# Kernel tuning notes

Measured on AMD Instinct MI355X. Metric: run time of the kernel, lower is better.

Reference implementation:

```python
import jax, jax.numpy as jnp
import numpy as np

NHEAD = 4
NLAYERS = 4
C = 128
EPS = 1e-5


def ln(x, g, b):
    m = x.mean(-1, keepdims=True)
    v = jnp.var(x, axis=-1, keepdims=True)
    return (x - m) / jnp.sqrt(v + EPS) * g + b


def mha_rel(q_in, k_in, in_w, in_b, out_w, out_b, pos_enc, pos_idx, self_attn):
    # q_in/k_in: [W, N, C]; pos_enc: [2W-1, C]; pos_idx: [W*W] int
    w, bsz, c = q_in.shape
    hd = c // NHEAD
    scale = hd ** -0.5
    if self_attn:
        qkv = q_in @ in_w.T + in_b
        q, k, v = jnp.split(qkv, 3, axis=-1)
    else:
        q = q_in @ in_w[:c].T + in_b[:c]
        kv = k_in @ in_w[c:].T + in_b[c:]
        k, v = jnp.split(kv, 2, axis=-1)
    pe = pos_enc[pos_idx].reshape(w, w, c)             # [W, W', C] gathered rel-pos
    qr_kr = pe @ in_w[:2 * c].T + in_b[:2 * c]
    q_r, k_r = jnp.split(qr_kr, 2, axis=-1)
    q = (q * scale).reshape(w, bsz, NHEAD, hd)
    q_r = (q_r * scale).reshape(w, w, NHEAD, hd)
    k = k.reshape(w, bsz, NHEAD, hd)
    v = v.reshape(w, bsz, NHEAD, hd)
    k_r = k_r.reshape(w, w, NHEAD, hd)
    # content-content + content-pos + pos-content (STTR MultiheadAttentionRelative)
    attn = (jnp.einsum('wnec,vnec->newv', q, k)
            + jnp.einsum('wnec,wvec->newv', q, k_r)
            + jnp.einsum('vnec,wvec->newv', k, q_r))   # [N, E, W, W']
    raw = attn.sum(1)
    a = jax.nn.softmax(attn, axis=-1)
    v_o = jnp.einsum('newv,vnec->wnec', a, v).reshape(w, bsz, c)
    v_o = v_o @ out_w.T + out_b
    return v_o, a.sum(1) / NHEAD, raw


def _forward(feat_left, feat_right, pos_enc,
             s_iw, s_ib, s_ow, s_ob, s_g, s_b,
             c_iw, c_ib, c_ow, c_ob, c_g1, c_b1, c_g2, c_b2):
    bs, c, hn0, w = feat_left.shape
    hn = hn0 * bs

    def to_seq(x):  # [bs,c,hn,w] -> [w, hn*bs, c]
        return jnp.transpose(jnp.transpose(x, (1, 3, 2, 0)).reshape(c, w, hn), (1, 2, 0))

    fl = to_seq(feat_left)
    fr = to_seq(feat_right)
    pos_idx = (jnp.arange(w - 1, -1, -1)[:, None] + jnp.arange(w)[None, :]).reshape(-1)
    pos_flip = pos_enc[::-1]
    feat = jnp.concatenate([fl, fr], axis=1)           # [w, 2hn, c]
    for i in range(NLAYERS):
        # self attention over concatenated left/right
        f2 = ln(feat, s_g[i], s_b[i])
        f2, _, _ = mha_rel(f2, f2, s_iw[i], s_ib[i], s_ow[i], s_ob[i], pos_enc, pos_idx, True)
        feat = feat + f2
        # cross attention
        fl, fr = feat[:, :hn], feat[:, hn:]
        fl2 = ln(fl, c_g1[i], c_b1[i])
        fr2 = ln(fr, c_g1[i], c_b1[i])
        fr2u, _, _ = mha_rel(fr2, fl2, c_iw[i], c_ib[i], c_ow[i], c_ob[i], pos_flip, pos_idx, False)
        fr = fr + fr2u
        fr2n = ln(fr, c_g2[i], c_b2[i])
        fl2u, _, _ = mha_rel(fl2, fr2n, c_iw[i], c_ib[i], c_ow[i], c_ob[i], pos_enc, pos_idx, False)
        fl = fl + fl2u
        feat = jnp.concatenate([fl, fr], axis=1)
    return feat


def setup_inputs() -> dict:
    key = jax.random.key(0)
    ks = jax.random.split(key, 20)
    bs, hn, w = 2, 64, 192
    p = 0.02
    return {
        "feat_left": jax.random.normal(ks[0], (bs, C, hn, w), jnp.float32),
        "feat_right": jax.random.normal(ks[1], (bs, C, hn, w), jnp.float32),
        "pos_enc": jax.random.normal(ks[2], (2 * w - 1, C), jnp.float32),
        "s_iw": jax.random.normal(ks[3], (NLAYERS, 3 * C, C), jnp.float32) * p,
        "s_ib": jax.random.normal(ks[4], (NLAYERS, 3 * C), jnp.float32) * p,
        "s_ow": jax.random.normal(ks[5], (NLAYERS, C, C), jnp.float32) * p,
        "s_ob": jax.random.normal(ks[6], (NLAYERS, C), jnp.float32) * p,
        "s_g": jnp.ones((NLAYERS, C), jnp.float32),
        "s_b": jnp.zeros((NLAYERS, C), jnp.float32),
        "c_iw": jax.random.normal(ks[7], (NLAYERS, 3 * C, C), jnp.float32) * p,
        "c_ib": jax.random.normal(ks[8], (NLAYERS, 3 * C), jnp.float32) * p,
        "c_ow": jax.random.normal(ks[9], (NLAYERS, C, C), jnp.float32) * p,
        "c_ob": jax.random.normal(ks[10], (NLAYERS, C), jnp.float32) * p,
        "c_g1": jnp.ones((NLAYERS, C), jnp.float32),
        "c_b1": jnp.zeros((NLAYERS, C), jnp.float32),
        "c_g2": jnp.ones((NLAYERS, C), jnp.float32),
        "c_b2": jnp.zeros((NLAYERS, C), jnp.float32),
    }


def reference(feat_left, feat_right, pos_enc,
              s_iw, s_ib, s_ow, s_ob, s_g, s_b,
              c_iw, c_ib, c_ow, c_ob, c_g1, c_b1, c_g2, c_b2):
    return _forward(feat_left, feat_right, pos_enc,
                    s_iw, s_ib, s_ow, s_ob, s_g, s_b,
                    c_iw, c_ib, c_ow, c_ob, c_g1, c_b1, c_g2, c_b2)
```

## Files before the change

kernel.cpp:

```cpp
#include <hip/hip_runtime.h>
#include <hip/hip_bf16.h>
#include <math.h>

#define WW 192
#define NTOT 256
#define HNN 128
#define CC 128
#define NH 4
#define NLAY 4
#define EPSF 1e-5f
#define SCALE 0.17677669529663687f

typedef __attribute__((ext_vector_type(8))) short short8_t;
typedef __attribute__((ext_vector_type(4))) float f32x4;

#define MFMA(a, b, c) __builtin_amdgcn_mfma_f32_16x16x32_bf16(a, b, c, 0, 0, 0)

__device__ __forceinline__ ushort f2b(float f) {
  union { float f; uint u; } x; x.f = f;
  uint r = x.u + 0x7fffu + ((x.u >> 16) & 1u);
  return (ushort)(r >> 16);
}

__global__ __launch_bounds__(256) void k_build_feat(const float* __restrict__ L,
                                                    const float* __restrict__ R,
                                                    float* __restrict__ feat) {
  __shared__ float tile[32][33];
  int wt = blockIdx.x, h0 = blockIdx.y, z = blockIdx.z;
  int ct = z & 3, b = (z >> 2) & 1, side = z >> 3;
  const float* src = side ? R : L;
  int tx = threadIdx.x & 31, ty = threadIdx.x >> 5;
  const float* sp = src + ((size_t)(b * 128 + ct * 32) * 64 + h0) * 192 + wt * 32;
  #pragma unroll
  for (int yy = 0; yy < 4; ++yy) {
    int c = ty * 4 + yy;
    tile[c][tx] = sp[(size_t)c * 64 * 192 + tx];
  }
  __syncthreads();
  int n = 2 * h0 + b + side * 128;
  #pragma unroll
  for (int yy = 0; yy < 4; ++yy) {
    int w = ty * 4 + yy;
    feat[((size_t)(wt * 32 + w) * 256 + n) * 128 + ct * 32 + tx] = tile[tx][w];
  }
}

__global__ __launch_bounds__(256) void k_wconv(
    const float* __restrict__ s_iw, const float* __restrict__ s_ow,
    const float* __restrict__ c_iw, const float* __restrict__ c_ow,
    ushort* __restrict__ out) {
  int i4 = (blockIdx.x * 256 + threadIdx.x) * 4;
  const float* src;
  int off;
  if (i4 < 196608) { src = s_iw; off = i4; }
  else if (i4 < 262144) { src = s_ow; off = i4 - 196608; }
  else if (i4 < 458752) { src = c_iw; off = i4 - 262144; }
  else { src = c_ow; off = i4 - 458752; }
  float4 v = *(const float4*)(src + off);
  ushort4 o;
  o.x = f2b(v.x); o.y = f2b(v.y); o.z = f2b(v.z); o.w = f2b(v.w);
  *(ushort4*)(out + i4) = o;
}

__global__ __launch_bounds__(256) void k_ln(const float* __restrict__ src,
                                            ushort* __restrict__ dst,
                                            const float* __restrict__ g,
                                            const float* __restrict__ b,
                                            int n0, int nsub) {
  int t = blockIdx.x * 4 + (threadIdx.x >> 6);
  int lane = threadIdx.x & 63;
  int w = t / nsub, h = t - w * nsub;
  size_t row = (size_t)(w * NTOT + n0 + h) * CC;
  int c0 = lane * 2;
  float2 x = *(const float2*)(src + row + c0);
  float s = x.x + x.y;
  float s2 = x.x * x.x + x.y * x.y;
  #pragma unroll
  for (int o = 1; o < 64; o <<= 1) {
    s += __shfl_xor(s, o);
    s2 += __shfl_xor(s2, o);
  }
  float m = s * (1.0f / 128.0f);
  float var = s2 * (1.0f / 128.0f) - m * m;
  float inv = rsqrtf(var + EPSF);
  float oa = (x.x - m) * inv * g[c0] + b[c0];
  float ob = (x.y - m) * inv * g[c0 + 1] + b[c0 + 1];
  uint pack = (uint)f2b(oa) | ((uint)f2b(ob) << 16);
  *(uint*)(dst + row + c0) = pack;
}

__global__ __launch_bounds__(256) void k_gemm_bf16(
    const ushort* __restrict__ X, int xN, int x0,
    const ushort* __restrict__ Wb, const float* __restrict__ bias,
    void* __restrict__ Yv, int yN, int y0, int ystride, int yf32res,
    int T, int nsub, float* __restrict__ Ymir) {
  extern __shared__ char smem[];
  ushort* As = (ushort*)smem;
  ushort* Bs = As + 128 * 128;
  float* biasS = (float*)(Bs + 128 * 128);

  int bm = blockIdx.x, bn = blockIdx.y;
  int tid = threadIdx.x;

  {
    int row = tid >> 1;
    int ce0 = (tid & 1) * 64;
    int t = bm * 128 + row;
    bool ok = (t < T);
    int w = 0, h = 0;
    if (ok) { w = t / nsub; h = t - w * nsub; }
    const ushort* src = X + (size_t)(w * xN + x0 + h) * CC + ce0;
    #pragma unroll
    for (int i = 0; i < 8; ++i) {
      short8_t v = {};
      if (ok) v = *(const short8_t*)(src + i * 8);
      int cb = (ce0 + i * 8) * 2;
      *(short8_t*)((char*)As + row * 256 + (cb ^ ((row & 7) << 4))) = v;
    }
    const ushort* wsrc = Wb + (size_t)(bn * 128 + row) * CC + ce0;
    #pragma unroll
    for (int i = 0; i < 8; ++i) {
      short8_t v = *(const short8_t*)(wsrc + i * 8);
      int cb = (ce0 + i * 8) * 2;
      *(short8_t*)((char*)Bs + row * 256 + (cb ^ ((row & 7) << 4))) = v;
    }
    if (tid < 128) biasS[tid] = bias[bn * 128 + tid];
  }
  __syncthreads();

  int lane = tid & 63, wid = tid >> 6;
  int wm = (wid >> 1) * 64, wn = (wid & 1) * 64;
  int r = lane & 15, g = lane >> 4;

  f32x4 acc[4][4] = {};
  #pragma unroll
  for (int kc = 0; kc < 4; ++kc) {
    short8_t af[4], bf[4];
    #pragma unroll
    for (int mt = 0; mt < 4; ++mt) {
      int row = wm + mt * 16 + r;
      af[mt] = *(const short8_t*)((const char*)As + row * 256 + ((kc * 64 + g * 16) ^ ((row & 7) << 4)));
    }
    #pragma unroll
    for (int nt = 0; nt < 4; ++nt) {
      int row = wn + nt * 16 + r;
      bf[nt] = *(const short8_t*)((const char*)Bs + row * 256 + ((kc * 64 + g * 16) ^ ((row & 7) << 4)));
    }
    __builtin_amdgcn_s_setprio(1);
    #pragma unroll
    for (int mt = 0; mt < 4; ++mt)
      #pragma unroll
      for (int nt = 0; nt < 4; ++nt)
        acc[mt][nt] = MFMA(af[mt], bf[nt], acc[mt][nt]);
    __builtin_amdgcn_s_setprio(0);
  }

  #pragma unroll
  for (int mt = 0; mt < 4; ++mt) {
    #pragma unroll
    for (int reg = 0; reg < 4; ++reg) {
      int t = bm * 128 + wm + mt * 16 + g * 4 + reg;
      if (t < T) {
        int w = t / nsub, h = t - w * nsub;
        size_t ybase = (size_t)(w * yN + y0 + h) * ystride + bn * 128;
        #pragma unroll
        for (int nt = 0; nt < 4; ++nt) {
          int nn = wn + nt * 16 + r;
          float v = acc[mt][nt][reg] + biasS[nn];
          if (yf32res) {
            float nv = ((float*)Yv)[ybase + nn] + v;
            ((float*)Yv)[ybase + nn] = nv;
            if (Ymir) Ymir[ybase + nn] = nv;
          } else {
            ((ushort*)Yv)[ybase + nn] = f2b(v);
          }
        }
      }
    }
  }
}

__global__ __launch_bounds__(256) void k_rr(
    const float* __restrict__ pos_enc,
    const float* __restrict__ s_iw, const float* __restrict__ s_ib,
    const float* __restrict__ c_iw, const float* __restrict__ c_ib,
    ushort* __restrict__ out_all) {
  extern __shared__ char smem[];
  ushort* As = (ushort*)smem;
  ushort* Bs = As + 128 * 128;
  float* biasS = (float*)(Bs + 128 * 128);

  int bm = blockIdx.x, bn = blockIdx.y, z = blockIdx.z;
  int layer = z >> 1;
  const float* Wt = ((z & 1) ? c_iw : s_iw) + (size_t)layer * 384 * CC;
  const float* bias = ((z & 1) ? c_ib : s_ib) + layer * 384;
  ushort* out = out_all + (size_t)z * 383 * 256;
  int tid = threadIdx.x;

  {
    int row = tid >> 1;
    int ce0 = (tid & 1) * 64;
    int t = bm * 128 + row;
    bool ok = (t < 383);
    const float* src = pos_enc + (size_t)t * CC + ce0;
    #pragma unroll
    for (int i = 0; i < 8; ++i) {
      float4 v0 = ok ? *(const float4*)(src + i * 8) : make_float4(0.f, 0.f, 0.f, 0.f);
      float4 v1 = ok ? *(const float4*)(src + i * 8 + 4) : make_float4(0.f, 0.f, 0.f, 0.f);
      short8_t pv;
      pv[0] = (short)f2b(v0.x); pv[1] = (short)f2b(v0.y);
      pv[2] = (short)f2b(v0.z); pv[3] = (short)f2b(v0.w);
      pv[4] = (short)f2b(v1.x); pv[5] = (short)f2b(v1.y);
      pv[6] = (short)f2b(v1.z); pv[7] = (short)f2b(v1.w);
      int cb = (ce0 + i * 8) * 2;
      *(short8_t*)((char*)As + row * 256 + (cb ^ ((row & 7) << 4))) = pv;
    }
    const float* wsrc = Wt + (size_t)(bn * 128 + row) * CC + ce0;
    #pragma unroll
    for (int i = 0; i < 8; ++i) {
      float4 v0 = *(const float4*)(wsrc + i * 8);
      float4 v1 = *(const float4*)(wsrc + i * 8 + 4);
      short8_t pv;
      pv[0] = (short)f2b(v0.x); pv[1] = (short)f2b(v0.y);
      pv[2] = (short)f2b(v0.z); pv[3] = (short)f2b(v0.w);
      pv[4] = (short)f2b(v1.x); pv[5] = (short)f2b(v1.y);
      pv[6] = (short)f2b(v1.z); pv[7] = (short)f2b(v1.w);
      int cb = (ce0 + i * 8) * 2;
      *(short8_t*)((char*)Bs + row * 256 + (cb ^ ((row & 7) << 4))) = pv;
    }
    if (tid < 128) biasS[tid] = bias[bn * 128 + tid];
  }
  __syncthreads();

  int lane = tid & 63, wid = tid >> 6;
  int wm = (wid >> 1) * 64, wn = (wid & 1) * 64;
  int r = lane & 15, g = lane >> 4;

  f32x4 acc[4][4] = {};
  #pragma unroll
  for (int kc = 0; kc < 4; ++kc) {
    short8_t af[4], bf[4];
    #pragma unroll
    for (int mt = 0; mt < 4; ++mt) {
      int row = wm + mt * 16 + r;
      af[mt] = *(const short8_t*)((const char*)As + row * 256 + ((kc * 64 + g * 16) ^ ((row & 7) << 4)));
    }
    #pragma unroll
    for (int nt = 0; nt < 4; ++nt) {
      int row = wn + nt * 16 + r;
      bf[nt] = *(const short8_t*)((const char*)Bs + row * 256 + ((kc * 64 + g * 16) ^ ((row & 7) << 4)));
    }
    #pragma unroll
    for (int mt = 0; mt < 4; ++mt)
      #pragma unroll
      for (int nt = 0; nt < 4; ++nt)
        acc[mt][nt] = MFMA(af[mt], bf[nt], acc[mt][nt]);
  }

  #pragma unroll
  for (int mt = 0; mt < 4; ++mt) {
    #pragma unroll
    for (int reg = 0; reg < 4; ++reg) {
      int t = bm * 128 + wm + mt * 16 + g * 4 + reg;
      if (t < 383) {
        #pragma unroll
        for (int nt = 0; nt < 4; ++nt) {
          int nn = wn + nt * 16 + r;
          out[(size_t)t * 256 + bn * 128 + nn] = f2b(acc[mt][nt][reg] + biasS[nn]);
        }
      }
    }
  }
}

#define KS_ST 36
#define VT_ST 196
#define B2_ST 37
#define PL_ST 20

template <int SGN>
__global__ __launch_bounds__(256, 4) void k_attn_mfma(
    const ushort* __restrict__ qbuf, int qstride, int qoff, int qN, int qn0,
    const ushort* __restrict__ kvbuf, int kvstride, int koff, int voff, int kN, int kn0,
    const ushort* __restrict__ rrb,
    ushort* __restrict__ obuf, int oN,
    int nblk) {
  __shared__ ushort Ks[192 * KS_ST];
  __shared__ ushort Vt[32 * VT_ST];
  __shared__ float Sb[4 * 16 * B2_ST];
  __shared__ uint PLb[4 * 16 * PL_ST];

  int bid = blockIdx.x;
  int n = bid % nblk;
  int rest = bid / nblk;
  int h = rest & 3;
  int ts = rest >> 2;
  int tid = threadIdx.x;
  int lane = tid & 63, wid = tid >> 6;
  int r = lane & 15, g = lane >> 4;
  int g4 = g * 4;

  for (int i = tid; i < 768; i += 256) {
    int row = i >> 2, c8 = (i & 3) * 8;
    *(short8_t*)&Ks[row * KS_ST + c8] =
        *(const short8_t*)(kvbuf + (size_t)(row * kN + kn0 + n) * kvstride + koff + h * 32 + c8);
  }
  {
    uint* Vtu = (uint*)Vt;
    for (int i = tid; i < 384; i += 256) {
      int dg = i / 96;
      int p = i - dg * 96;
      const ushort* vb = kvbuf + (size_t)((2 * p) * kN + kn0 + n) * kvstride + voff + h * 32 + dg * 8;
      short8_t a = *(const short8_t*)vb;
      short8_t b = *(const short8_t*)(vb + (size_t)kN * kvstride);
      #pragma unroll
      for (int j = 0; j < 8; ++j)
        Vtu[(dg * 8 + j) * 98 + p] = ((uint)(ushort)a[j]) | (((uint)(ushort)b[j]) << 16);
    }
  }
  int w0 = (ts * 4 + wid) * 16;
  short8_t qf = *(const short8_t*)(qbuf + (size_t)((w0 + r) * qN + qn0 + n) * qstride + qoff + h * 32 + g * 8);
  __syncthreads();

  float* flat = Sb + wid * 16 * B2_ST;
  uint* PL = PLb + wid * 16 * PL_ST;
  const ushort* KRg = rrb + 128 + h * 32 + g * 8;
  const ushort* QRg = rrb + h * 32 + g * 8;
  const f32x4 zf = {0.f, 0.f, 0.f, 0.f};

  int ca = (SGN < 0) ? (r + 1) : (31 - r);
  int cbn = (SGN < 0) ? (17 + r) : (15 - r);
  int rdcol = 16 - r + g4;

  f32x4 esum = zf, o0 = zf, o1 = zf;

  #pragma unroll
  for (int vp = 0; vp < 6; ++vp) {
    #pragma unroll
    for (int half = 0; half < 2; ++half) {
      int s = 2 * vp + half;
      int v0 = s * 16;
      short8_t kf = *(const short8_t*)&Ks[(v0 + r) * KS_ST + g * 8];
      int base2 = 176 + SGN * (w0 - v0);
      const ushort* krp = KRg + (size_t)(base2 + r) * 256;
      const ushort* qrp = QRg + (size_t)(base2 + r) * 256;
      short8_t krf0 = *(const short8_t*)krp;
      short8_t krf1 = *(const short8_t*)(krp + 16 * 256);
      short8_t qrf0 = *(const short8_t*)qrp;
      short8_t qrf1 = *(const short8_t*)(qrp + 16 * 256);
      __builtin_amdgcn_s_setprio(1);
      f32x4 t1  = MFMA(kf, qf, zf);
      f32x4 t3a = MFMA(kf, qrf0, zf);
      f32x4 t3b = MFMA(kf, qrf1, zf);
      f32x4 t2a = MFMA(qf, krf0, zf);
      f32x4 t2b = MFMA(qf, krf1, zf);
      __builtin_amdgcn_s_setprio(0);
      #pragma unroll
      for (int reg = 0; reg < 4; ++reg) {
        flat[(g4 + reg) * B2_ST + ca] = t2a[reg];
        flat[(g4 + reg) * B2_ST + cbn] = t2b[reg];
      }
      f32x4 p2v = *(const f32x4*)&flat[r * B2_ST + rdcol];
      f32x4 ev;
      #pragma unroll
      for (int reg = 0; reg < 4; ++reg) {
        int js = 15 + SGN * (r - g4 - reg);
        int idx = (lane & 48) | (js & 15);
        float v3a = __shfl(t3a[reg], idx);
        float v3b = __shfl(t3b[reg], idx);
        float p3 = (js < 16) ? v3a : v3b;
        float e = __expf((t1[reg] + p2v[reg] + p3) * SCALE);
        ev[reg] = e;
        esum[reg] += e;
      }
      uint pa = (uint)f2b(ev[0]) | ((uint)f2b(ev[1]) << 16);
      uint pbu = (uint)f2b(ev[2]) | ((uint)f2b(ev[3]) << 16);
      *(uint2*)&PL[r * PL_ST + 8 * half + 2 * g] = make_uint2(pa, pbu);
    }
    union { uint u[4]; short8_t s8; } pb;
    uint4 pr = *(const uint4*)&PL[r * PL_ST + 4 * g];
    pb.u[0] = pr.x; pb.u[1] = pr.y; pb.u[2] = pr.z; pb.u[3] = pr.w;
    short8_t vt0 = *(const short8_t*)&Vt[r * VT_ST + vp * 32 + g * 8];
    short8_t vt1 = *(const short8_t*)&Vt[(16 + r) * VT_ST + vp * 32 + g * 8];
    __builtin_amdgcn_s_setprio(1);
    o0 = MFMA(vt0, pb.s8, o0);
    o1 = MFMA(vt1, pb.s8, o1);
    __builtin_amdgcn_s_setprio(0);
  }

  float ssum = (esum[0] + esum[1]) + (esum[2] + esum[3]);
  ssum += __shfl_xor(ssum, 16);
  ssum += __shfl_xor(ssum, 32);

  float inv = 1.0f / ssum;
  ushort4 u0, u1;
  u0.x = f2b(o0[0] * inv); u0.y = f2b(o0[1] * inv);
  u0.z = f2b(o0[2] * inv); u0.w = f2b(o0[3] * inv);
  u1.x = f2b(o1[0] * inv); u1.y = f2b(o1[1] * inv);
  u1.z = f2b(o1[2] * inv); u1.w = f2b(o1[3] * inv);
  size_t rowb = (size_t)((w0 + r) * oN + n) * CC + h * 32;
  *(ushort4*)(obuf + rowb + g4) = u0;
  *(ushort4*)(obuf + rowb + 16 + g4) = u1;
}

extern "C" void kernel_launch(void* const* d_in, const int* in_sizes, int n_in,
                              void* d_out, int out_size, void* d_ws, size_t ws_size,
                              hipStream_t stream) {
  const float* feat_left  = (const float*)d_in[0];
  const float* feat_right = (const float*)d_in[1];
  const float* pos_enc    = (const float*)d_in[2];
  const float* s_iw = (const float*)d_in[3];
  const float* s_ib = (const float*)d_in[4];
  const float* s_ow = (const float*)d_in[5];
  const float* s_ob = (const float*)d_in[6];
  const float* s_g  = (const float*)d_in[7];
  const float* s_b  = (const float*)d_in[8];
  const float* c_iw = (const float*)d_in[9];
  const float* c_ib = (const float*)d_in[10];
  const float* c_ow = (const float*)d_in[11];
  const float* c_ob = (const float*)d_in[12];
  const float* c_g1 = (const float*)d_in[13];
  const float* c_b1 = (const float*)d_in[14];
  const float* c_g2 = (const float*)d_in[15];
  const float* c_b2 = (const float*)d_in[16];

  char* W = (char*)d_ws;
  const int FEAT_N = WW * NTOT * CC;
  float*  feat    = (float*)W;
  ushort* f2obuf  = (ushort*)(W + 25165824);
  ushort* qkv     = (ushort*)(W + 37748736);
  ushort* kv2     = (ushort*)(W + 75497472);
  ushort* rrb_all = (ushort*)(W + 88080384);
  ushort* wbf     = (ushort*)(W + 89649152);

  ushort* f2   = f2obuf;
  ushort* obuf = f2obuf;

  const int GEMM_LDS = 128 * 128 * 2 * 2 + 128 * 4;
  hipFuncSetAttribute(reinterpret_cast<const void*>(&k_gemm_bf16),
                      hipFuncAttributeMaxDynamicSharedMemorySize, GEMM_LDS);
  hipFuncSetAttribute(reinterpret_cast<const void*>(&k_rr),
                      hipFuncAttributeMaxDynamicSharedMemorySize, GEMM_LDS);

  k_build_feat<<<dim3(6, 64, 16), 256, 0, stream>>>(feat_left, feat_right, feat);
  k_rr<<<dim3(3, 2, 8), 256, GEMM_LDS, stream>>>(pos_enc, s_iw, s_ib, c_iw, c_ib, rrb_all);
  k_wconv<<<512, 256, 0, stream>>>(s_iw, s_ow, c_iw, c_ow, wbf);

  const ushort* siw_bf_base = wbf;
  const ushort* sow_bf_base = wbf + 196608;
  const ushort* ciw_bf_base = wbf + 262144;
  const ushort* cow_bf_base = wbf + 458752;

  const int T_FULL = WW * NTOT;
  const int T_HALF = WW * HNN;

  for (int i = 0; i < NLAY; ++i) {
    const float* sib = s_ib + i * 384;
    const float* sob = s_ob + i * CC;
    const float* cib = c_ib + i * 384;
    const float* cob = c_ob + i * CC;
    const ushort* siw_bf = siw_bf_base + (size_t)i * 384 * CC;
    const ushort* sow_bf = sow_bf_base + (size_t)i * CC * CC;
    const ushort* ciw_bf = ciw_bf_base + (size_t)i * 384 * CC;
    const ushort* cow_bf = cow_bf_base + (size_t)i * CC * CC;
    const ushort* rr_self  = rrb_all + (size_t)(2 * i) * 383 * 256;
    const ushort* rr_cross = rrb_all + (size_t)(2 * i + 1) * 383 * 256;
    float* mir = (i == NLAY - 1) ? (float*)d_out : nullptr;

    k_ln<<<T_FULL / 4, 256, 0, stream>>>(feat, f2, s_g + i * CC, s_b + i * CC, 0, NTOT);
    k_gemm_bf16<<<dim3(T_FULL / 128, 3), 256, GEMM_LDS, stream>>>(
        f2, NTOT, 0, siw_bf, sib, qkv, NTOT, 0, 384, 0, T_FULL, NTOT, nullptr);
    k_attn_mfma<-1><<<NTOT * NH * 3, 256, 0, stream>>>(
        qkv, 384, 0, NTOT, 0, qkv, 384, 128, 256, NTOT, 0,
        rr_self, obuf, NTOT, NTOT);
    k_gemm_bf16<<<dim3(T_FULL / 128, 1), 256, GEMM_LDS, stream>>>(
        obuf, NTOT, 0, sow_bf, sob, feat, NTOT, 0, CC, 1, T_FULL, NTOT, nullptr);

    k_ln<<<T_FULL / 4, 256, 0, stream>>>(feat, f2, c_g1 + i * CC, c_b1 + i * CC, 0, NTOT);
    k_gemm_bf16<<<dim3(T_FULL / 128, 3), 256, GEMM_LDS, stream>>>(
        f2, NTOT, 0, ciw_bf, cib, qkv, NTOT, 0, 384, 0, T_FULL, NTOT, nullptr);

    k_attn_mfma<+1><<<HNN * NH * 3, 256, 0, stream>>>(
        qkv, 384, 0, NTOT, 128, qkv, 384, 128, 256, NTOT, 0,
        rr_cross, obuf, HNN, HNN);
    k_gemm_bf16<<<dim3(T_HALF / 128, 1), 256, GEMM_LDS, stream>>>(
        obuf, HNN, 0, cow_bf, cob, feat, NTOT, 128, CC, 1, T_HALF, HNN, mir);

    k_ln<<<T_HALF / 4, 256, 0, stream>>>(feat, f2, c_g2 + i * CC, c_b2 + i * CC, 128, HNN);
    k_gemm_bf16<<<dim3(T_HALF / 128, 2), 256, GEMM_LDS, stream>>>(
        f2, NTOT, 128, ciw_bf + 128 * CC, cib + 128, kv2, HNN, 0, 256, 0, T_HALF, HNN, nullptr);
    k_attn_mfma<-1><<<HNN * NH * 3, 256, 0, stream>>>(
        qkv, 384, 0, NTOT, 0, kv2, 256, 0, 128, HNN, 0,
        rr_cross, obuf, HNN, HNN);
    k_gemm_bf16<<<dim3(T_HALF / 128, 1), 256, GEMM_LDS, stream>>>(
        obuf, HNN, 0, cow_bf, cob, feat, NTOT, 0, CC, 1, T_HALF, HNN, mir);
  }
}
```

Baseline: 1.382 ms.

## Fuse out-projection residual with following LayerNorms; batch two sequences per attention block

Adds a k_gemm_out kernel that performs the output projection, adds the residual into feat, and computes the row LayerNorm(s) for the next stage in its epilogue, emitting bf16 inputs for one or two subsequent GEMMs. This removes the separate k_ln launches and their extra read of feat, and moves the next layer's self-attention LN into the previous layer's last output GEMM. The self-attention kernel now processes two batch columns per block to amortise setup and cut grid size, and the GEMM drops its bounds checks. The costs are extra buffers, more register pressure in the fused epilogue, and less parallelism in self-attention.

```diff
diff --git a/kernel.cpp b/kernel.cpp
--- a/kernel.cpp
+++ b/kernel.cpp
@@ -92,8 +92,8 @@
 __global__ __launch_bounds__(256) void k_gemm_bf16(
     const ushort* __restrict__ X, int xN, int x0,
     const ushort* __restrict__ Wb, const float* __restrict__ bias,
-    void* __restrict__ Yv, int yN, int y0, int ystride, int yf32res,
-    int T, int nsub, float* __restrict__ Ymir) {
+    ushort* __restrict__ Y, int yN, int y0, int ystride,
+    int T, int nsub) {
   extern __shared__ char smem[];
   ushort* As = (ushort*)smem;
   ushort* Bs = As + 128 * 128;
@@ -106,14 +106,11 @@
     int row = tid >> 1;
     int ce0 = (tid & 1) * 64;
     int t = bm * 128 + row;
-    bool ok = (t < T);
-    int w = 0, h = 0;
-    if (ok) { w = t / nsub; h = t - w * nsub; }
+    int w = t / nsub, h = t - w * nsub;
     const ushort* src = X + (size_t)(w * xN + x0 + h) * CC + ce0;
     #pragma unroll
     for (int i = 0; i < 8; ++i) {
-      short8_t v = {};
-      if (ok) v = *(const short8_t*)(src + i * 8);
+      short8_t v = *(const short8_t*)(src + i * 8);
       int cb = (ce0 + i * 8) * 2;
       *(short8_t*)((char*)As + row * 256 + (cb ^ ((row & 7) << 4))) = v;
     }
@@ -160,21 +157,147 @@
     #pragma unroll
     for (int reg = 0; reg < 4; ++reg) {
       int t = bm * 128 + wm + mt * 16 + g * 4 + reg;
-      if (t < T) {
-        int w = t / nsub, h = t - w * nsub;
-        size_t ybase = (size_t)(w * yN + y0 + h) * ystride + bn * 128;
-        #pragma unroll
-        for (int nt = 0; nt < 4; ++nt) {
-          int nn = wn + nt * 16 + r;
-          float v = acc[mt][nt][reg] + biasS[nn];
-          if (yf32res) {
-            float nv = ((float*)Yv)[ybase + nn] + v;
-            ((float*)Yv)[ybase + nn] = nv;
-            if (Ymir) Ymir[ybase + nn] = nv;
-          } else {
-            ((ushort*)Yv)[ybase + nn] = f2b(v);
-          }
-        }
+      int w = t / nsub, h = t - w * nsub;
+      size_t ybase = (size_t)(w * yN + y0 + h) * ystride + bn * 128;
+      #pragma unroll
+      for (int nt = 0; nt < 4; ++nt) {
+        int nn = wn + nt * 16 + r;
+        Y[ybase + nn] = f2b(acc[mt][nt][reg] + biasS[nn]);
+      }
+    }
+  }
+}
+
+__global__ __launch_bounds__(256) void k_gemm_out(
+    const ushort* __restrict__ X, int xN,
+    const ushort* __restrict__ Wb, const float* __restrict__ bias,
+    float* __restrict__ Y, int y0, float* __restrict__ Ymir,
+    const float* __restrict__ g1, const float* __restrict__ b1,
+    ushort* __restrict__ dst1, int d1N, int d1n0,
+    const float* __restrict__ g2, const float* __restrict__ b2,
+    ushort* __restrict__ dst2, int d2N, int d2n0,
+    int T, int nsub) {
+  extern __shared__ char smem[];
+  ushort* As = (ushort*)smem;
+  ushort* Bs = As + 128 * 128;
+  float* biasS = (float*)(Bs + 128 * 128);
+  float* rsum = biasS + 128;
+  float* rsq  = rsum + 256;
+
+  int bm = blockIdx.x;
+  int tid = threadIdx.x;
+
+  {
+    int row = tid >> 1;
+    int ce0 = (tid & 1) * 64;
+    int t = bm * 128 + row;
+    int w = t / nsub, h = t - w * nsub;
+    const ushort* src = X + (size_t)(w * xN + h) * CC + ce0;
+    #pragma unroll
+    for (int i = 0; i < 8; ++i) {
+      short8_t v = *(const short8_t*)(src + i * 8);
+      int cb = (ce0 + i * 8) * 2;
+      *(short8_t*)((char*)As + row * 256 + (cb ^ ((row & 7) << 4))) = v;
+    }
+    const ushort* wsrc = Wb + (size_t)row * CC + ce0;
+    #pragma unroll
+    for (int i = 0; i < 8; ++i) {
+      short8_t v = *(const short8_t*)(wsrc + i * 8);
+      int cb = (ce0 + i * 8) * 2;
+      *(short8_t*)((char*)Bs + row * 256 + (cb ^ ((row & 7) << 4))) = v;
+    }
+    if (tid < 128) biasS[tid] = bias[tid];
+  }
+  __syncthreads();
+
+  int lane = tid & 63, wid = tid >> 6;
+  int wm = (wid >> 1) * 64, wn = (wid & 1) * 64;
+  int r = lane & 15, g = lane >> 4;
+  int g4 = g * 4;
+
+  f32x4 acc[4][4] = {};
+  #pragma unroll
+  for (int kc = 0; kc < 4; ++kc) {
+    short8_t af[4], bf[4];
+    #pragma unroll
+    for (int mt = 0; mt < 4; ++mt) {
+      int row = wm + mt * 16 + r;
+      af[mt] = *(const short8_t*)((const char*)As + row * 256 + ((kc * 64 + g * 16) ^ ((row & 7) << 4)));
+    }
+    #pragma unroll
+    for (int nt = 0; nt < 4; ++nt) {
+      int row = wn + nt * 16 + r;
+      bf[nt] = *(const short8_t*)((const char*)Bs + row * 256 + ((kc * 64 + g * 16) ^ ((row & 7) << 4)));
+    }
+    __builtin_amdgcn_s_setprio(1);
+    #pragma unroll
+    for (int mt = 0; mt < 4; ++mt)
+      #pragma unroll
+      for (int nt = 0; nt < 4; ++nt)
+        acc[mt][nt] = MFMA(af[mt], bf[nt], acc[mt][nt]);
+    __builtin_amdgcn_s_setprio(0);
+  }
+
+  float nvv[4][4][4];
+  #pragma unroll
+  for (int mt = 0; mt < 4; ++mt) {
+    #pragma unroll
+    for (int reg = 0; reg < 4; ++reg) {
+      int rloc = wm + mt * 16 + g4 + reg;
+      int t = bm * 128 + rloc;
+      int w = t / nsub, h = t - w * nsub;
+      size_t ybase = (size_t)(w * NTOT + y0 + h) * CC;
+      float s = 0.f, q = 0.f;
+      #pragma unroll
+      for (int nt = 0; nt < 4; ++nt) {
+        int nn = wn + nt * 16 + r;
+        float nv = Y[ybase + nn] + acc[mt][nt][reg] + biasS[nn];
+        Y[ybase + nn] = nv;
+        if (Ymir) Ymir[ybase + nn] = nv;
+        nvv[mt][reg][nt] = nv;
+        s += nv;
+        q += nv * nv;
+      }
+      #pragma unroll
+      for (int o = 1; o < 16; o <<= 1) {
+        s += __shfl_xor(s, o);
+        q += __shfl_xor(q, o);
+      }
+      if (r == 0) {
+        rsum[rloc * 2 + (wn >> 6)] = s;
+        rsq[rloc * 2 + (wn >> 6)] = q;
+      }
+    }
+  }
+  if (!dst1) return;
+  __syncthreads();
+
+  float g1c[4], b1c[4], g2c[4], b2c[4];
+  #pragma unroll
+  for (int nt = 0; nt < 4; ++nt) {
+    int nn = wn + nt * 16 + r;
+    g1c[nt] = g1[nn]; b1c[nt] = b1[nn];
+    if (dst2) { g2c[nt] = g2[nn]; b2c[nt] = b2[nn]; }
+  }
+  #pragma unroll
+  for (int mt = 0; mt < 4; ++mt) {
+    #pragma unroll
+    for (int reg = 0; reg < 4; ++reg) {
+      int rloc = wm + mt * 16 + g4 + reg;
+      int t = bm * 128 + rloc;
+      int w = t / nsub, h = t - w * nsub;
+      float S = rsum[rloc * 2] + rsum[rloc * 2 + 1];
+      float Q = rsq[rloc * 2] + rsq[rloc * 2 + 1];
+      float m = S * (1.0f / 128.0f);
+      float inv = rsqrtf(Q * (1.0f / 128.0f) - m * m + EPSF);
+      size_t d1base = (size_t)(w * d1N + d1n0 + h) * CC;
+      size_t d2base = dst2 ? (size_t)(w * d2N + d2n0 + h) * CC : 0;
+      #pragma unroll
+      for (int nt = 0; nt < 4; ++nt) {
+        int nn = wn + nt * 16 + r;
+        float xn = (nvv[mt][reg][nt] - m) * inv;
+        dst1[d1base + nn] = f2b(xn * g1c[nt] + b1c[nt]);
+        if (dst2) dst2[d2base + nn] = f2b(xn * g2c[nt] + b2c[nt]);
       }
     }
   }
@@ -278,7 +401,7 @@
 #define B2_ST 37
 #define PL_ST 20
 
-template <int SGN>
+template <int SGN, int NGRP>
 __global__ __launch_bounds__(256, 4) void k_attn_mfma(
     const ushort* __restrict__ qbuf, int qstride, int qoff, int qN, int qn0,
     const ushort* __restrict__ kvbuf, int kvstride, int koff, int voff, int kN, int kn0,
@@ -291,8 +414,9 @@
   __shared__ uint PLb[4 * 16 * PL_ST];
 
   int bid = blockIdx.x;
-  int n = bid % nblk;
-  int rest = bid / nblk;
+  int nb2 = nblk / NGRP;
+  int n0 = (bid % nb2) * NGRP;
+  int rest = bid / nb2;
   int h = rest & 3;
   int ts = rest >> 2;
   int tid = threadIdx.x;
@@ -300,28 +424,6 @@
   int r = lane & 15, g = lane >> 4;
   int g4 = g * 4;
 
-  for (int i = tid; i < 768; i += 256) {
-    int row = i >> 2, c8 = (i & 3) * 8;
-    *(short8_t*)&Ks[row * KS_ST + c8] =
-        *(const short8_t*)(kvbuf + (size_t)(row * kN + kn0 + n) * kvstride + koff + h * 32 + c8);
-  }
-  {
-    uint* Vtu = (uint*)Vt;
-    for (int i = tid; i < 384; i += 256) {
-      int dg = i / 96;
-      int p = i - dg * 96;
-      const ushort* vb = kvbuf + (size_t)((2 * p) * kN + kn0 + n) * kvstride + voff + h * 32 + dg * 8;
-      short8_t a = *(const short8_t*)vb;
-      short8_t b = *(const short8_t*)(vb + (size_t)kN * kvstride);
-      #pragma unroll
-      for (int j = 0; j < 8; ++j)
-        Vtu[(dg * 8 + j) * 98 + p] = ((uint)(ushort)a[j]) | (((uint)(ushort)b[j]) << 16);
-    }
-  }
-  int w0 = (ts * 4 + wid) * 16;
-  short8_t qf = *(const short8_t*)(qbuf + (size_t)((w0 + r) * qN + qn0 + n) * qstride + qoff + h * 32 + g * 8);
-  __syncthreads();
-
   float* flat = Sb + wid * 16 * B2_ST;
   uint* PL = PLb + wid * 16 * PL_ST;
   const ushort* KRg = rrb + 128 + h * 32 + g * 8;
@@ -331,76 +433,102 @@
   int ca = (SGN < 0) ? (r + 1) : (31 - r);
   int cbn = (SGN < 0) ? (17 + r) : (15 - r);
   int rdcol = 16 - r + g4;
-
-  f32x4 esum = zf, o0 = zf, o1 = zf;
-
-  #pragma unroll
-  for (int vp = 0; vp < 6; ++vp) {
-    #pragma unroll
-    for (int half = 0; half < 2; ++half) {
-      int s = 2 * vp + half;
-      int v0 = s * 16;
-      short8_t kf = *(const short8_t*)&Ks[(v0 + r) * KS_ST + g * 8];
-      int base2 = 176 + SGN * (w0 - v0);
-      const ushort* krp = KRg + (size_t)(base2 + r) * 256;
-      const ushort* qrp = QRg + (size_t)(base2 + r) * 256;
-      short8_t krf0 = *(const short8_t*)krp;
-      short8_t krf1 = *(const short8_t*)(krp + 16 * 256);
-      short8_t qrf0 = *(const short8_t*)qrp;
-      short8_t qrf1 = *(const short8_t*)(qrp + 16 * 256);
+  int w0 = (ts * 4 + wid) * 16;
+
+  for (int ni = 0; ni < NGRP; ++ni) {
+    int n = n0 + ni;
+    if (ni) __syncthreads();
+    for (int i = tid; i < 768; i += 256) {
+      int row = i >> 2, c8 = (i & 3) * 8;
+      *(short8_t*)&Ks[row * KS_ST + c8] =
+          *(const short8_t*)(kvbuf + (size_t)(row * kN + kn0 + n) * kvstride + koff + h * 32 + c8);
+    }
+    {
+      uint* Vtu = (uint*)Vt;
+      for (int i = tid; i < 384; i += 256) {
+        int dg = i / 96;
+        int p = i - dg * 96;
+        const ushort* vb = kvbuf + (size_t)((2 * p) * kN + kn0 + n) * kvstride + voff + h * 32 + dg * 8;
+        short8_t a = *(const short8_t*)vb;
+        short8_t b = *(const short8_t*)(vb + (size_t)kN * kvstride);
+        #pragma unroll
+        for (int j = 0; j < 8; ++j)
+          Vtu[(dg * 8 + j) * 98 + p] = ((uint)(ushort)a[j]) | (((uint)(ushort)b[j]) << 16);
+      }
+    }
+    short8_t qf = *(const short8_t*)(qbuf + (size_t)((w0 + r) * qN + qn0 + n) * qstride + qoff + h * 32 + g * 8);
+    __syncthreads();
+
+    f32x4 esum = zf, o0 = zf, o1 = zf;
+
+    #pragma unroll
+    for (int vp = 0; vp < 6; ++vp) {
+      #pragma unroll
+      for (int half = 0; half < 2; ++half) {
+        int s = 2 * vp + half;
+        int v0 = s * 16;
+        short8_t kf = *(const short8_t*)&Ks[(v0 + r) * KS_ST + g * 8];
+        int base2 = 176 + SGN * (w0 - v0);
+        const ushort* krp = KRg + (size_t)(base2 + r) * 256;
+        const ushort* qrp = QRg + (size_t)(base2 + r) * 256;
+        short8_t krf0 = *(const short8_t*)krp;
+        short8_t krf1 = *(const short8_t*)(krp + 16 * 256);
+        short8_t qrf0 = *(const short8_t*)qrp;
+        short8_t qrf1 = *(const short8_t*)(qrp + 16 * 256);
+        __builtin_amdgcn_s_setprio(1);
+        f32x4 t1  = MFMA(kf, qf, zf);
+        f32x4 t3a = MFMA(kf, qrf0, zf);
+        f32x4 t3b = MFMA(kf, qrf1, zf);
+        f32x4 t2a = MFMA(qf, krf0, zf);
+        f32x4 t2b = MFMA(qf, krf1, zf);
+        __builtin_amdgcn_s_setprio(0);
+        #pragma unroll
+        for (int reg = 0; reg < 4; ++reg) {
+          flat[(g4 + reg) * B2_ST + ca] = t2a[reg];
+          flat[(g4 + reg) * B2_ST + cbn] = t2b[reg];
+        }
+        f32x4 p2v = *(const f32x4*)&flat[r * B2_ST + rdcol];
+        f32x4 ev;
+        #pragma unroll
+        for (int reg = 0; reg < 4; ++reg) {
+          int js = 15 + SGN * (r - g4 - reg);
+          int idx = (lane & 48) | (js & 15);
+          float v3a = __shfl(t3a[reg], idx);
+          float v3b = __shfl(t3b[reg], idx);
+          float p3 = (js < 16) ? v3a : v3b;
+          float e = __expf((t1[reg] + p2v[reg] + p3) * SCALE);
+          ev[reg] = e;
+          esum[reg] += e;
+        }
+        uint pa = (uint)f2b(ev[0]) | ((uint)f2b(ev[1]) << 16);
+        uint pbu = (uint)f2b(ev[2]) | ((uint)f2b(ev[3]) << 16);
+        *(uint2*)&PL[r * PL_ST + 8 * half + 2 * g] = make_uint2(pa, pbu);
+      }
+      union { uint u[4]; short8_t s8; } pb;
+      uint4 pr = *(const uint4*)&PL[r * PL_ST + 4 * g];
+      pb.u[0] = pr.x; pb.u[1] = pr.y; pb.u[2] = pr.z; pb.u[3] = pr.w;
+      short8_t vt0 = *(const short8_t*)&Vt[r * VT_ST + vp * 32 + g * 8];
+      short8_t vt1 = *(const short8_t*)&Vt[(16 + r) * VT_ST + vp * 32 + g * 8];
       __builtin_amdgcn_s_setprio(1);
-      f32x4 t1  = MFMA(kf, qf, zf);
-      f32x4 t3a = MFMA(kf, qrf0, zf);
-      f32x4 t3b = MFMA(kf, qrf1, zf);
-      f32x4 t2a = MFMA(qf, krf0, zf);
-      f32x4 t2b = MFMA(qf, krf1, zf);
+      o0 = MFMA(vt0, pb.s8, o0);
+      o1 = MFMA(vt1, pb.s8, o1);
       __builtin_amdgcn_s_setprio(0);
-      #pragma unroll
-      for (int reg = 0; reg < 4; ++reg) {
-        flat[(g4 + reg) * B2_ST + ca] = t2a[reg];
-        flat[(g4 + reg) * B2_ST + cbn] = t2b[reg];
-      }
-      f32x4 p2v = *(const f32x4*)&flat[r * B2_ST + rdcol];
-      f32x4 ev;
-      #pragma unroll
-      for (int reg = 0; reg < 4; ++reg) {
-        int js = 15 + SGN * (r - g4 - reg);
-        int idx = (lane & 48) | (js & 15);
-        float v3a = __shfl(t3a[reg], idx);
-        float v3b = __shfl(t3b[reg], idx);
-        float p3 = (js < 16) ? v3a : v3b;
-        float e = __expf((t1[reg] + p2v[reg] + p3) * SCALE);
-        ev[reg] = e;
-        esum[reg] += e;
-      }
-      uint pa = (uint)f2b(ev[0]) | ((uint)f2b(ev[1]) << 16);
-      uint pbu = (uint)f2b(ev[2]) | ((uint)f2b(ev[3]) << 16);
-      *(uint2*)&PL[r * PL_ST + 8 * half + 2 * g] = make_uint2(pa, pbu);
-    }
-    union { uint u[4]; short8_t s8; } pb;
-    uint4 pr = *(const uint4*)&PL[r * PL_ST + 4 * g];
-    pb.u[0] = pr.x; pb.u[1] = pr.y; pb.u[2] = pr.z; pb.u[3] = pr.w;
-    short8_t vt0 = *(const short8_t*)&Vt[r * VT_ST + vp * 32 + g * 8];
-    short8_t vt1 = *(const short8_t*)&Vt[(16 + r) * VT_ST + vp * 32 + g * 8];
-    __builtin_amdgcn_s_setprio(1);
-    o0 = MFMA(vt0, pb.s8, o0);
-    o1 = MFMA(vt1, pb.s8, o1);
-    __builtin_amdgcn_s_setprio(0);
-  }
-
-  float ssum = (esum[0] + esum[1]) + (esum[2] + esum[3]);
-  ssum += __shfl_xor(ssum, 16);
-  ssum += __shfl_xor(ssum, 32);
-
-  float inv = 1.0f / ssum;
-  ushort4 u0, u1;
-  u0.x = f2b(o0[0] * inv); u0.y = f2b(o0[1] * inv);
-  u0.z = f2b(o0[2] * inv); u0.w = f2b(o0[3] * inv);
-  u1.x = f2b(o1[0] * inv); u1.y = f2b(o1[1] * inv);
-  u1.z = f2b(o1[2] * inv); u1.w = f2b(o1[3] * inv);
-  size_t rowb = (size_t)((w0 + r) * oN + n) * CC + h * 32;
-  *(ushort4*)(obuf + rowb + g4) = u0;
-  *(ushort4*)(obuf + rowb + 16 + g4) = u1;
+    }
+
+    float ssum = (esum[0] + esum[1]) + (esum[2] + esum[3]);
+    ssum += __shfl_xor(ssum, 16);
+    ssum += __shfl_xor(ssum, 32);
+
+    float inv = 1.0f / ssum;
+    ushort4 u0, u1;
+    u0.x = f2b(o0[0] * inv); u0.y = f2b(o0[1] * inv);
+    u0.z = f2b(o0[2] * inv); u0.w = f2b(o0[3] * inv);
+    u1.x = f2b(o1[0] * inv); u1.y = f2b(o1[1] * inv);
+    u1.z = f2b(o1[2] * inv); u1.w = f2b(o1[3] * inv);
+    size_t rowb = (size_t)((w0 + r) * oN + n) * CC + h * 32;
+    *(ushort4*)(obuf + rowb + g4) = u0;
+    *(ushort4*)(obuf + rowb + 16 + g4) = u1;
+  }
 }
 
 extern "C" void kernel_launch(void* const* d_in, const int* in_sizes, int n_in,
@@ -425,20 +553,23 @@
   const float* c_b2 = (const float*)d_in[16];
 
   char* W = (char*)d_ws;
-  const int FEAT_N = WW * NTOT * CC;
   float*  feat    = (float*)W;
-  ushort* f2obuf  = (ushort*)(W + 25165824);
+  ushort* f2s     = (ushort*)(W + 25165824);
   ushort* qkv     = (ushort*)(W + 37748736);
-  ushort* kv2     = (ushort*)(W + 75497472);
-  ushort* rrb_all = (ushort*)(W + 88080384);
-  ushort* wbf     = (ushort*)(W + 89649152);
-
-  ushort* f2   = f2obuf;
-  ushort* obuf = f2obuf;
+  ushort* obuf    = (ushort*)(W + 75497472);
+  ushort* kv2     = (ushort*)(W + 88080384);
+  ushort* rrb_all = (ushort*)(W + 100663296);
+  ushort* wbf     = (ushort*)(W + 102232064);
+
+  ushort* f2c1 = f2s;
+  ushort* f2c2 = obuf + WW * HNN * CC;
 
   const int GEMM_LDS = 128 * 128 * 2 * 2 + 128 * 4;
+  const int OUT_LDS  = 128 * 128 * 2 * 2 + 128 * 4 + 2048;
   hipFuncSetAttribute(reinterpret_cast<const void*>(&k_gemm_bf16),
                       hipFuncAttributeMaxDynamicSharedMemorySize, GEMM_LDS);
+  hipFuncSetAttribute(reinterpret_cast<const void*>(&k_gemm_out),
+                      hipFuncAttributeMaxDynamicSharedMemorySize, OUT_LDS);
   hipFuncSetAttribute(reinterpret_cast<const void*>(&k_rr),
                       hipFuncAttributeMaxDynamicSharedMemorySize, GEMM_LDS);
 
@@ -453,6 +584,8 @@
 
   const int T_FULL = WW * NTOT;
   const int T_HALF = WW * HNN;
+
+  k_ln<<<T_FULL / 4, 256, 0, stream>>>(feat, f2s, s_g, s_b, 0, NTOT);
 
   for (int i = 0; i < NLAY; ++i) {
     const float* sib = s_ib + i * 384;
@@ -465,34 +598,38 @@
     const ushort* cow_bf = cow_bf_base + (size_t)i * CC * CC;
     const ushort* rr_self  = rrb_all + (size_t)(2 * i) * 383 * 256;
     const ushort* rr_cross = rrb_all + (size_t)(2 * i + 1) * 383 * 256;
-    float* mir = (i == NLAY - 1) ? (float*)d_out : nullptr;
-
-    k_ln<<<T_FULL / 4, 256, 0, stream>>>(feat, f2, s_g + i * CC, s_b + i * CC, 0, NTOT);
+    int last = (i == NLAY - 1);
+    float* mir = last ? (float*)d_out : nullptr;
+    const float* sg_n = s_g + (i + 1) * CC;
+    const float* sb_n = s_b + (i + 1) * CC;
+
     k_gemm_bf16<<<dim3(T_FULL / 128, 3), 256, GEMM_LDS, stream>>>(
-        f2, NTOT, 0, siw_bf, sib, qkv, NTOT, 0, 384, 0, T_FULL, NTOT, nullptr);
-    k_attn_mfma<-1><<<NTOT * NH * 3, 256, 0, stream>>>(
+        f2s, NTOT, 0, siw_bf, sib, qkv, NTOT, 0, 384, T_FULL, NTOT);
+    k_attn_mfma<-1, 2><<<(NTOT / 2) * NH * 3, 256, 0, stream>>>(
         qkv, 384, 0, NTOT, 0, qkv, 384, 128, 256, NTOT, 0,
         rr_self, obuf, NTOT, NTOT);
-    k_gemm_bf16<<<dim3(T_FULL / 128, 1), 256, GEMM_LDS, stream>>>(
-        obuf, NTOT, 0, sow_bf, sob, feat, NTOT, 0, CC, 1, T_FULL, NTOT, nullptr);
-
-    k_ln<<<T_FULL / 4, 256, 0, stream>>>(feat, f2, c_g1 + i * CC, c_b1 + i * CC, 0, NTOT);
+    k_gemm_out<<<T_FULL / 128, 256, OUT_LDS, stream>>>(
+        obuf, NTOT, sow_bf, sob, feat, 0, nullptr,
+        c_g1 + i * CC, c_b1 + i * CC, f2c1, NTOT, 0,
+        nullptr, nullptr, nullptr, 0, 0, T_FULL, NTOT);
     k_gemm_bf16<<<dim3(T_FULL / 128, 3), 256, GEMM_LDS, stream>>>(
-        f2, NTOT, 0, ciw_bf, cib, qkv, NTOT, 0, 384, 0, T_FULL, NTOT, nullptr);
-
-    k_attn_mfma<+1><<<HNN * NH * 3, 256, 0, stream>>>(
+        f2c1, NTOT, 0, ciw_bf, cib, qkv, NTOT, 0, 384, T_FULL, NTOT);
+    k_attn_mfma<+1, 1><<<HNN * NH * 3, 256, 0, stream>>>(
         qkv, 384, 0, NTOT, 128, qkv, 384, 128, 256, NTOT, 0,
         rr_cross, obuf, HNN, HNN);
-    k_gemm_bf16<<<dim3(T_HALF / 128, 1), 256, GEMM_LDS, stream>>>(
-        obuf, HNN, 0, cow_bf, cob, feat, NTOT, 128, CC, 1, T_HALF, HNN, mir);
-
-    k_ln<<<T_HALF / 4, 256, 0, stream>>>(feat, f2, c_g2 + i * CC, c_b2 + i * CC, 128, HNN);
+    k_gemm_out<<<T_HALF / 128, 256, OUT_LDS, stream>>>(
+        obuf, HNN, cow_bf, cob, feat, 128, mir,
+        c_g2 + i * CC, c_b2 + i * CC, f2c2, HNN, 0,
+        last ? nullptr : sg_n, sb_n, last ? nullptr : f2s, NTOT, 128,
+        T_HALF, HNN);
     k_gemm_bf16<<<dim3(T_HALF / 128, 2), 256, GEMM_LDS, stream>>>(
-        f2, NTOT, 128, ciw_bf + 128 * CC, cib + 128, kv2, HNN, 0, 256, 0, T_HALF, HNN, nullptr);
-    k_attn_mfma<-1><<<HNN * NH * 3, 256, 0, stream>>>(
+        f2c2, HNN, 0, ciw_bf + 128 * CC, cib + 128, kv2, HNN, 0, 256, T_HALF, HNN);
+    k_attn_mfma<-1, 1><<<HNN * NH * 3, 256, 0, stream>>>(
         qkv, 384, 0, NTOT, 0, kv2, 256, 0, 128, HNN, 0,
         rr_cross, obuf, HNN, HNN);
-    k_gemm_bf16<<<dim3(T_HALF / 128, 1), 256, GEMM_LDS, stream>>>(
-        obuf, HNN, 0, cow_bf, cob, feat, NTOT, 0, CC, 1, T_HALF, HNN, mir);
-  }
-}
+    k_gemm_out<<<T_HALF / 128, 256, OUT_LDS, stream>>>(
+        obuf, HNN, cow_bf, cob, feat, 0, mir,
+        last ? nullptr : sg_n, sb_n, last ? nullptr : f2s, NTOT, 0,
+        nullptr, nullptr, nullptr, 0, 0, T_HALF, HNN);
+  }
+}
```

Measured after the change: 1.609 ms. 16.5% more time.
